# Kernel tuning notes

Measured on AMD Instinct MI355X. Metric: run time of the kernel, lower is better.

Reference implementation:

```python
import jax, jax.numpy as jnp
import numpy as np

B, T, D, H = 4, 2048, 512, 8
DH = D // H


def setup_inputs() -> dict:
    key = jax.random.key(0)
    ks = jax.random.split(key, 13)
    s = 1.0 / np.sqrt(D)
    inp = {
        "q": jax.random.normal(ks[0], (B, T, D), jnp.float32),
        "k": jax.random.normal(ks[1], (B, T, D), jnp.float32),
        "v": jax.random.normal(ks[2], (B, T, D), jnp.float32),
        # key padding mask, broadcastable to [B, H, T_q, T_k]; mostly True
        "padding_mask": jax.random.uniform(ks[3], (B, 1, 1, T)) > 0.1,
        "W_q": jax.random.normal(ks[4], (D, D), jnp.float32) * s,
        "b_q": jnp.zeros((D,), jnp.float32),
        "W_k": jax.random.normal(ks[5], (D, D), jnp.float32) * s,
        "b_k": jnp.zeros((D,), jnp.float32),
        "W_v": jax.random.normal(ks[6], (D, D), jnp.float32) * s,
        "b_v": jnp.zeros((D,), jnp.float32),
        "W_o": jax.random.normal(ks[7], (D, D), jnp.float32) * s,
        "b_o": jnp.zeros((D,), jnp.float32),
    }
    return inp


def reference(q, k, v, padding_mask, W_q, b_q, W_k, b_k, W_v, b_v, W_o, b_o):
    # Linear projections, then split heads: [B, T, D] -> [B, H, T, DH]
    def heads(x, W, b):
        y = x @ W + b
        return y.reshape(x.shape[0], x.shape[1], H, DH).transpose(0, 2, 1, 3)

    Q = heads(q, W_q, b_q)
    K = heads(k, W_k, b_k)
    V = heads(v, W_v, b_v)

    scores = jnp.einsum("bhqd,bhkd->bhqk", Q, K) / jnp.sqrt(jnp.float32(DH))
    scores = jnp.where(padding_mask, scores, -jnp.inf)
    weights = jax.nn.softmax(scores, axis=-1)
    weights = jnp.nan_to_num(weights, nan=0.0)  # all-masked rows -> 0
    x = jnp.einsum("bhqk,bhkd->bhqd", weights, V)
    x = x.transpose(0, 2, 1, 3).reshape(q.shape[0], q.shape[1], D)
    return x @ W_o + b_o
```

## Files before the change

### kernel.cpp

```cpp
#include <hip/hip_runtime.h>
#include <hip/hip_bf16.h>
#include <math.h>


#define TB 2048
#define DD 512
#define NH 8
#define DH 64

typedef short bf16x8 __attribute__((ext_vector_type(8)));
typedef float f32x4 __attribute__((ext_vector_type(4)));

static __device__ __forceinline__ ushort f2bf(float x) {
  __hip_bfloat16 h = __float2bfloat16(x);
  return *reinterpret_cast<ushort*>(&h);
}
static __device__ __forceinline__ float bf2f(ushort u) {
  unsigned int v = ((unsigned int)u) << 16;
  return __uint_as_float(v);
}
static __device__ __forceinline__ float fast_exp2(float x) {
  return __builtin_amdgcn_exp2f(x);
}
static __device__ __forceinline__ unsigned pack2(float x, float y) {
  return __builtin_amdgcn_perm(__float_as_uint(y) + 0x8000u,
                               __float_as_uint(x) + 0x8000u, 0x07060302u);
}
static __device__ __forceinline__ bf16x8 cvt8(float4 lo, float4 hi) {
  union { unsigned u[4]; bf16x8 v; } r;
  r.u[0] = pack2(lo.x, lo.y);
  r.u[1] = pack2(lo.z, lo.w);
  r.u[2] = pack2(hi.x, hi.y);
  r.u[3] = pack2(hi.z, hi.w);
  return r.v;
}

__global__ void mask_detect_kernel(const unsigned char* __restrict__ m,
                                   int* __restrict__ mode) {
  __shared__ int c1, c2;
  if (threadIdx.x == 0) { c1 = 0; c2 = 0; }
  __syncthreads();
  int l1 = 0, l2 = 0;
  for (int i = threadIdx.x; i < 8192; i += blockDim.x) {
    int ph = i & 3;
    unsigned char v = m[i];
    if (ph == 1 && v) l1++;
    if (ph == 2 && v) l2++;
  }
  if (l1) atomicAdd(&c1, l1);
  if (l2) atomicAdd(&c2, l2);
  __syncthreads();
  if (threadIdx.x == 0) *mode = (c1 > 0) ? 0 : ((c2 > 0) ? 1 : 2);
}

__global__ void mask_build_kernel(const void* __restrict__ m,
                                  const int* __restrict__ mode,
                                  float* __restrict__ out) {
  int i = blockIdx.x * blockDim.x + threadIdx.x;
  int md = *mode;
  int v;
  if (md == 0)      v = ((const unsigned char*)m)[i] != 0;
  else if (md == 1) v = ((const float*)m)[i] != 0.0f;
  else              v = ((const int*)m)[i] != 0;
  out[i] = v ? 0.0f : -INFINITY;
}

__global__ __launch_bounds__(256) void wtrans3_kernel(
    const float* __restrict__ Wq, const float* __restrict__ Wk,
    const float* __restrict__ Wv, ushort* __restrict__ Wall) {
  __shared__ ushort t[64][68];
  const float* W = (blockIdx.z == 0) ? Wq : (blockIdx.z == 1) ? Wk : Wv;
  ushort* Wt = Wall + (size_t)blockIdx.z * (512 * 512);
  const int bn = blockIdx.x << 6, bk = blockIdx.y << 6;
  const int tx = threadIdx.x & 15, ty = threadIdx.x >> 4;
#pragma unroll
  for (int rr = 0; rr < 64; rr += 16) {
    float4 v = *(const float4*)&W[(size_t)(bk + rr + ty) * DD + bn + (tx << 2)];
    t[(tx << 2) + 0][rr + ty] = f2bf(v.x);
    t[(tx << 2) + 1][rr + ty] = f2bf(v.y);
    t[(tx << 2) + 2][rr + ty] = f2bf(v.z);
    t[(tx << 2) + 3][rr + ty] = f2bf(v.w);
  }
  __syncthreads();
#pragma unroll
  for (int rr = 0; rr < 64; rr += 16) {
    ushort4 o;
    o.x = t[rr + ty][(tx << 2) + 0];
    o.y = t[rr + ty][(tx << 2) + 1];
    o.z = t[rr + ty][(tx << 2) + 2];
    o.w = t[rr + ty][(tx << 2) + 3];
    *(ushort4*)&Wt[(size_t)(bn + rr + ty) * DD + bk + (tx << 2)] = o;
  }
}

__global__ __launch_bounds__(256) void wtrans_split_kernel(
    const float* __restrict__ W, ushort* __restrict__ Wt) {
  __shared__ ushort thi[64][68];
  __shared__ ushort tlo[64][68];
  const int bn = blockIdx.x << 6, bk = blockIdx.y << 6;
  const int tx = threadIdx.x & 15, ty = threadIdx.x >> 4;
#pragma unroll
  for (int rr = 0; rr < 64; rr += 16) {
    float4 v = *(const float4*)&W[(size_t)(bk + rr + ty) * DD + bn + (tx << 2)];
    float vv[4] = {v.x, v.y, v.z, v.w};
#pragma unroll
    for (int c = 0; c < 4; ++c) {
      ushort hi = f2bf(vv[c]);
      ushort lo = f2bf(vv[c] - bf2f(hi));
      thi[(tx << 2) + c][rr + ty] = hi;
      tlo[(tx << 2) + c][rr + ty] = lo;
    }
  }
  __syncthreads();
#pragma unroll
  for (int rr = 0; rr < 64; rr += 16) {
    ushort4 h4, l4;
    h4.x = thi[rr + ty][(tx << 2) + 0];
    h4.y = thi[rr + ty][(tx << 2) + 1];
    h4.z = thi[rr + ty][(tx << 2) + 2];
    h4.w = thi[rr + ty][(tx << 2) + 3];
    l4.x = tlo[rr + ty][(tx << 2) + 0];
    l4.y = tlo[rr + ty][(tx << 2) + 1];
    l4.z = tlo[rr + ty][(tx << 2) + 2];
    l4.w = tlo[rr + ty][(tx << 2) + 3];
    size_t rowb = (size_t)(bn + rr + ty) * 1536;
    *(ushort4*)&Wt[rowb + bk + (tx << 2)] = h4;
    *(ushort4*)&Wt[rowb + 512 + bk + (tx << 2)] = h4;
    *(ushort4*)&Wt[rowb + 1024 + bk + (tx << 2)] = l4;
  }
}

__global__ __launch_bounds__(256) void projqkv_kernel(
    const float* __restrict__ Qx, const float* __restrict__ Kx,
    const float* __restrict__ Vx, const ushort* __restrict__ Wall,
    const float* __restrict__ bq, const float* __restrict__ bk,
    const float* __restrict__ bv, ushort* __restrict__ Yall, float qscale) {
  __shared__ __align__(16) ushort As[2][128][32];
  __shared__ __align__(16) ushort Bs[2][128][32];

  const int tid = threadIdx.x;
  const int w = tid >> 6, lane = tid & 63;
  const int llo = lane & 15, lhi = lane >> 4;
  const int wm = w >> 1, wn = w & 1;

  const int bid = blockIdx.x;
  const int x = bid & 7, rest = bid >> 3;
  const int ni = rest & 3;
  const int gg = (rest >> 2) * 8 + x;
  const int sec = gg >> 6;
  const int mt = gg & 63;
  const int m0 = mt << 7;
  const int n0s = ni << 7;

  const float* A = (sec == 0) ? Qx : (sec == 1) ? Kx : Vx;
  const float* bias = (sec == 0) ? bq : (sec == 1) ? bk : bv;
  const float scale = (sec == 0) ? qscale : 1.0f;
  const ushort* Wt = Wall + (size_t)(sec * 512 + n0s) * DD;

  const int srow = tid >> 1, scol = (tid & 1) << 4;
  const float* Ag = A + (size_t)(m0 + srow) * DD + scol;
  const ushort* Bg = Wt + (size_t)srow * DD + scol;

  f32x4 acc[4][4];
#pragma unroll
  for (int mi = 0; mi < 4; ++mi)
#pragma unroll
    for (int nj = 0; nj < 4; ++nj) acc[mi][nj] = (f32x4){0.f, 0.f, 0.f, 0.f};

  {
    float4 f0 = *(const float4*)(Ag + 0);
    float4 f1 = *(const float4*)(Ag + 4);
    float4 f2 = *(const float4*)(Ag + 8);
    float4 f3 = *(const float4*)(Ag + 12);
    bf16x8 w0 = *(const bf16x8*)(Bg + 0);
    bf16x8 w1 = *(const bf16x8*)(Bg + 8);
    *(bf16x8*)&As[0][srow][scol] = cvt8(f0, f1);
    *(bf16x8*)&As[0][srow][scol + 8] = cvt8(f2, f3);
    *(bf16x8*)&Bs[0][srow][scol] = w0;
    *(bf16x8*)&Bs[0][srow][scol + 8] = w1;
  }
  __syncthreads();

  int cur = 0;
  for (int t = 0; t < 16; ++t) {
    float4 f0, f1, f2, f3;
    bf16x8 w0, w1;
    if (t < 15) {
      const float* ag = Ag + (t + 1) * 32;
      const ushort* bg = Bg + (t + 1) * 32;
      f0 = *(const float4*)(ag + 0);
      f1 = *(const float4*)(ag + 4);
      f2 = *(const float4*)(ag + 8);
      f3 = *(const float4*)(ag + 12);
      w0 = *(const bf16x8*)(bg + 0);
      w1 = *(const bf16x8*)(bg + 8);
    }
    bf16x8 af[4], bfr[4];
#pragma unroll
    for (int mi = 0; mi < 4; ++mi)
      af[mi] = *(const bf16x8*)&As[cur][wm * 64 + mi * 16 + llo][lhi * 8];
#pragma unroll
    for (int nj = 0; nj < 4; ++nj)
      bfr[nj] = *(const bf16x8*)&Bs[cur][wn * 64 + nj * 16 + llo][lhi * 8];
    __builtin_amdgcn_s_setprio(1);
#pragma unroll
    for (int mi = 0; mi < 4; ++mi)
#pragma unroll
      for (int nj = 0; nj < 4; ++nj)
        acc[mi][nj] = __builtin_amdgcn_mfma_f32_16x16x32_bf16(
            af[mi], bfr[nj], acc[mi][nj], 0, 0, 0);
    __builtin_amdgcn_s_setprio(0);
    if (t < 15) {
      *(bf16x8*)&As[cur ^ 1][srow][scol] = cvt8(f0, f1);
      *(bf16x8*)&As[cur ^ 1][srow][scol + 8] = cvt8(f2, f3);
      *(bf16x8*)&Bs[cur ^ 1][srow][scol] = w0;
      *(bf16x8*)&Bs[cur ^ 1][srow][scol + 8] = w1;
    }
    __syncthreads();
    cur ^= 1;
  }

  float bb[4];
#pragma unroll
  for (int nj = 0; nj < 4; ++nj)
    bb[nj] = bias[n0s + wn * 64 + nj * 16 + llo];

  ushort* Yq = Yall;
  ushort* Yk = Yall + ((size_t)4 << 20);
  ushort* Yv = Yall + ((size_t)8 << 20);
#pragma unroll
  for (int mi = 0; mi < 4; ++mi)
#pragma unroll
    for (int nj = 0; nj < 4; ++nj) {
      int colS = n0s + wn * 64 + nj * 16 + llo;
      int h = colS >> 6, dh = colS & (DH - 1);
#pragma unroll
      for (int r = 0; r < 4; ++r) {
        int row = m0 + wm * 64 + mi * 16 + lhi * 4 + r;
        int bidx = row >> 11, t = row & (TB - 1);
        int bh = bidx * NH + h;
        ushort u = f2bf((acc[mi][nj][r] + bb[nj]) * scale);
        if (sec == 0) {
          Yq[((size_t)(bh * 128 + (t >> 4)) * 2 + (dh >> 5)) * 512 +
             ((((dh >> 3) & 3) << 4) + (t & 15)) * 8 + (dh & 7)] = u;
        } else if (sec == 1) {
          Yk[((size_t)(bh * 32 + (t >> 6)) << 12) +
             (((dh >> 5) << 2) + ((t >> 4) & 3)) * 512 +
             ((((dh >> 3) & 3) << 4) + (t & 15)) * 8 + (dh & 7)] = u;
        } else {
          Yv[((size_t)(bh * 32 + (t >> 6)) << 12) +
             ((((t >> 5) & 1) << 2) + (dh >> 4)) * 512 +
             ((((t >> 3) & 3) << 4) + (dh & 15)) * 8 + (t & 7)] = u;
        }
      }
    }
}

__global__ __launch_bounds__(256) void projo_kernel(
    const ushort* __restrict__ A, const ushort* __restrict__ Wt,
    const float* __restrict__ bias, float* __restrict__ Y) {
  __shared__ __align__(16) ushort As[2][128][32];
  __shared__ __align__(16) ushort Bs[2][64][32];

  const int tid = threadIdx.x;
  const int w = tid >> 6, lane = tid & 63;
  const int llo = lane & 15, lhi = lane >> 4;
  const int wm = w >> 1, wn = w & 1;

  const int bid = blockIdx.x;
  const int x = bid & 7, rest = bid >> 3;
  const int ni = rest & 7;
  const int mt = (rest >> 3) * 8 + x;
  const int m0 = mt << 7;
  const int n0 = ni << 6;
  const int K = 1536;

  const int arow = tid >> 1, acol = (tid & 1) << 4;
  const int brow = tid >> 2, bcol = (tid & 3) << 3;
  const ushort* Ag = A + (size_t)(m0 + arow) * K + acol;
  const ushort* Bg = Wt + (size_t)(n0 + brow) * K + bcol;

  f32x4 acc[4][2];
#pragma unroll
  for (int mi = 0; mi < 4; ++mi)
#pragma unroll
    for (int nj = 0; nj < 2; ++nj) acc[mi][nj] = (f32x4){0.f, 0.f, 0.f, 0.f};

  {
    bf16x8 a0 = *(const bf16x8*)(Ag + 0);
    bf16x8 a1 = *(const bf16x8*)(Ag + 8);
    bf16x8 b0 = *(const bf16x8*)(Bg + 0);
    *(bf16x8*)&As[0][arow][acol] = a0;
    *(bf16x8*)&As[0][arow][acol + 8] = a1;
    *(bf16x8*)&Bs[0][brow][bcol] = b0;
  }
  __syncthreads();

  int cur = 0;
#pragma unroll 2
  for (int t = 0; t < 48; ++t) {
    bf16x8 a0, a1, b0;
    if (t < 47) {
      const ushort* ag = Ag + (t + 1) * 32;
      const ushort* bg = Bg + (t + 1) * 32;
      a0 = *(const bf16x8*)(ag + 0);
      a1 = *(const bf16x8*)(ag + 8);
      b0 = *(const bf16x8*)(bg + 0);
    }
    bf16x8 af[4], bfr[2];
#pragma unroll
    for (int mi = 0; mi < 4; ++mi)
      af[mi] = *(const bf16x8*)&As[cur][wm * 64 + mi * 16 + llo][lhi * 8];
#pragma unroll
    for (int nj = 0; nj < 2; ++nj)
      bfr[nj] = *(const bf16x8*)&Bs[cur][wn * 32 + nj * 16 + llo][lhi * 8];
    __builtin_amdgcn_s_setprio(1);
#pragma unroll
    for (int mi = 0; mi < 4; ++mi)
#pragma unroll
      for (int nj = 0; nj < 2; ++nj)
        acc[mi][nj] = __builtin_amdgcn_mfma_f32_16x16x32_bf16(
            af[mi], bfr[nj], acc[mi][nj], 0, 0, 0);
    __builtin_amdgcn_s_setprio(0);
    if (t < 47) {
      *(bf16x8*)&As[cur ^ 1][arow][acol] = a0;
      *(bf16x8*)&As[cur ^ 1][arow][acol + 8] = a1;
      *(bf16x8*)&Bs[cur ^ 1][brow][bcol] = b0;
    }
    __syncthreads();
    cur ^= 1;
  }

  float bb[2];
#pragma unroll
  for (int nj = 0; nj < 2; ++nj)
    bb[nj] = bias[n0 + wn * 32 + nj * 16 + llo];
#pragma unroll
  for (int mi = 0; mi < 4; ++mi)
#pragma unroll
    for (int nj = 0; nj < 2; ++nj) {
      int col = n0 + wn * 32 + nj * 16 + llo;
#pragma unroll
      for (int r = 0; r < 4; ++r) {
        int row = m0 + wm * 64 + mi * 16 + lhi * 4 + r;
        Y[(size_t)row * DD + col] = acc[mi][nj][r] + bb[nj];
      }
    }
}

__global__ __launch_bounds__(256) void attn_mfma_kernel(
    const ushort* __restrict__ Qf,
    const ushort* __restrict__ Kf,
    const ushort* __restrict__ Vf,
    const float* __restrict__ mbias,
    ushort* __restrict__ Ap) {
  __shared__ __align__(16) ushort Plds[4][2][16][72];

  const int tid = threadIdx.x;
  const int w = tid >> 6, lane = tid & 63;
  const int lhi = lane >> 4, llo = lane & 15;
  const int lane8 = lane * 8;

  const int bid = blockIdx.x;
  const int j = bid >> 3;
  const int bh = (bid & 7) + ((j >> 4) << 3);
  const int qt = j & 15;
  const int b = bh >> 3, h = bh & 7;
  const int q0 = qt << 7;

  const float* mb = mbias + b * TB;
  ushort* plA = &Plds[w][0][0][0];
  ushort* plB = &Plds[w][1][0][0];

  const ushort* Qb =
      Qf + ((size_t)((bh << 7) + (q0 >> 4) + w * 2) * 2) * 512 + lane8;
  bf16x8 qa0 = *(const bf16x8*)Qb;
  bf16x8 qa1 = *(const bf16x8*)(Qb + 512);
  bf16x8 qa2 = *(const bf16x8*)(Qb + 1024);
  bf16x8 qa3 = *(const bf16x8*)(Qb + 1536);

  const size_t bhK = (size_t)bh << 5;
  f32x4 oaccA[4], oaccB[4];
#pragma unroll
  for (int nt = 0; nt < 4; ++nt) {
    oaccA[nt] = (f32x4){0.f, 0.f, 0.f, 0.f};
    oaccB[nt] = (f32x4){0.f, 0.f, 0.f, 0.f};
  }
  float mA = -INFINITY, lA = 0.f;
  float mB = -INFINITY, lB = 0.f;

  for (int kt64 = 0; kt64 < 32; ++kt64) {
    const ushort* Kt = Kf + ((bhK + kt64) << 12) + lane8;
    bf16x8 kf[8];
#pragma unroll
    for (int i = 0; i < 8; ++i) kf[i] = *(const bf16x8*)(Kt + i * 512);
    float4 mb4[4];
#pragma unroll
    for (int nt = 0; nt < 4; ++nt)
      mb4[nt] = *(const float4*)&mb[kt64 * 64 + nt * 16 + lhi * 4];

    f32x4 sA[4], sB[4];
    __builtin_amdgcn_s_setprio(1);
#pragma unroll
    for (int nt = 0; nt < 4; ++nt) {
      sA[nt] = (f32x4){0.f, 0.f, 0.f, 0.f};
      sA[nt] = __builtin_amdgcn_mfma_f32_16x16x32_bf16(kf[nt], qa0, sA[nt], 0, 0, 0);
      sA[nt] = __builtin_amdgcn_mfma_f32_16x16x32_bf16(kf[4 + nt], qa1, sA[nt], 0, 0, 0);
    }
#pragma unroll
    for (int nt = 0; nt < 4; ++nt) {
      sB[nt] = (f32x4){0.f, 0.f, 0.f, 0.f};
      sB[nt] = __builtin_amdgcn_mfma_f32_16x16x32_bf16(kf[nt], qa2, sB[nt], 0, 0, 0);
      sB[nt] = __builtin_amdgcn_mfma_f32_16x16x32_bf16(kf[4 + nt], qa3, sB[nt], 0, 0, 0);
    }
    __builtin_amdgcn_s_setprio(0);

    const ushort* Vt = Vf + ((bhK + kt64) << 12) + lane8;
    bf16x8 vf[8];
#pragma unroll
    for (int i = 0; i < 8; ++i) vf[i] = *(const bf16x8*)(Vt + i * 512);

#pragma unroll
    for (int nt = 0; nt < 4; ++nt) {
      sA[nt][0] += mb4[nt].x; sB[nt][0] += mb4[nt].x;
      sA[nt][1] += mb4[nt].y; sB[nt][1] += mb4[nt].y;
      sA[nt][2] += mb4[nt].z; sB[nt][2] += mb4[nt].z;
      sA[nt][3] += mb4[nt].w; sB[nt][3] += mb4[nt].w;
    }

    {
      float mx0 = fmaxf(fmaxf(sA[0][0], sA[0][1]), fmaxf(sA[0][2], sA[0][3]));
      float mx1 = fmaxf(fmaxf(sA[1][0], sA[1][1]), fmaxf(sA[1][2], sA[1][3]));
      float mx2 = fmaxf(fmaxf(sA[2][0], sA[2][1]), fmaxf(sA[2][2], sA[2][3]));
      float mx3 = fmaxf(fmaxf(sA[3][0], sA[3][1]), fmaxf(sA[3][2], sA[3][3]));
      float lmax = fmaxf(fmaxf(mx0, mx1), fmaxf(mx2, mx3));
      if (__any(lmax > mA + 8.f)) {
        float rmax = fmaxf(lmax, __shfl_xor(lmax, 16));
        rmax = fmaxf(rmax, __shfl_xor(rmax, 32));
        float newm = fmaxf(mA, rmax);
        float alpha = (newm == -INFINITY) ? 0.f : fast_exp2(mA - newm);
        float al[4];
#pragma unroll
        for (int r = 0; r < 4; ++r) al[r] = __shfl(alpha, lhi * 4 + r);
#pragma unroll
        for (int nt = 0; nt < 4; ++nt) {
          oaccA[nt][0] *= al[0];
          oaccA[nt][1] *= al[1];
          oaccA[nt][2] *= al[2];
          oaccA[nt][3] *= al[3];
        }
        lA *= alpha;
        mA = newm;
      }
#pragma unroll
      for (int nt = 0; nt < 4; ++nt)
#pragma unroll
        for (int r = 0; r < 4; ++r) sA[nt][r] = fast_exp2(sA[nt][r] - mA);
      if (__any(mA == -INFINITY)) {
        if (mA == -INFINITY) {
#pragma unroll
          for (int nt = 0; nt < 4; ++nt) sA[nt] = (f32x4){0.f, 0.f, 0.f, 0.f};
        }
      }
      float s0 = (sA[0][0] + sA[0][1]) + (sA[0][2] + sA[0][3]);
      float s1 = (sA[1][0] + sA[1][1]) + (sA[1][2] + sA[1][3]);
      float s2 = (sA[2][0] + sA[2][1]) + (sA[2][2] + sA[2][3]);
      float s3 = (sA[3][0] + sA[3][1]) + (sA[3][2] + sA[3][3]);
      lA += (s0 + s1) + (s2 + s3);
#pragma unroll
      for (int nt = 0; nt < 4; ++nt) {
        unsigned int lo = pack2(sA[nt][0], sA[nt][1]);
        unsigned int hi = pack2(sA[nt][2], sA[nt][3]);
        *(uint2*)&plA[llo * 72 + nt * 16 + lhi * 4] = make_uint2(lo, hi);
      }
    }

    {
      float mx0 = fmaxf(fmaxf(sB[0][0], sB[0][1]), fmaxf(sB[0][2], sB[0][3]));
      float mx1 = fmaxf(fmaxf(sB[1][0], sB[1][1]), fmaxf(sB[1][2], sB[1][3]));
      float mx2 = fmaxf(fmaxf(sB[2][0], sB[2][1]), fmaxf(sB[2][2], sB[2][3]));
      float mx3 = fmaxf(fmaxf(sB[3][0], sB[3][1]), fmaxf(sB[3][2], sB[3][3]));
      float lmax = fmaxf(fmaxf(mx0, mx1), fmaxf(mx2, mx3));
      if (__any(lmax > mB + 8.f)) {
        float rmax = fmaxf(lmax, __shfl_xor(lmax, 16));
        rmax = fmaxf(rmax, __shfl_xor(rmax, 32));
        float newm = fmaxf(mB, rmax);
        float alpha = (newm == -INFINITY) ? 0.f : fast_exp2(mB - newm);
        float al[4];
#pragma unroll
        for (int r = 0; r < 4; ++r) al[r] = __shfl(alpha, lhi * 4 + r);
#pragma unroll
        for (int nt = 0; nt < 4; ++nt) {
          oaccB[nt][0] *= al[0];
          oaccB[nt][1] *= al[1];
          oaccB[nt][2] *= al[2];
          oaccB[nt][3] *= al[3];
        }
        lB *= alpha;
        mB = newm;
      }
#pragma unroll
      for (int nt = 0; nt < 4; ++nt)
#pragma unroll
        for (int r = 0; r < 4; ++r) sB[nt][r] = fast_exp2(sB[nt][r] - mB);
      if (__any(mB == -INFINITY)) {
        if (mB == -INFINITY) {
#pragma unroll
          for (int nt = 0; nt < 4; ++nt) sB[nt] = (f32x4){0.f, 0.f, 0.f, 0.f};
        }
      }
      float s0 = (sB[0][0] + sB[0][1]) + (sB[0][2] + sB[0][3]);
      float s1 = (sB[1][0] + sB[1][1]) + (sB[1][2] + sB[1][3]);
      float s2 = (sB[2][0] + sB[2][1]) + (sB[2][2] + sB[2][3]);
      float s3 = (sB[3][0] + sB[3][1]) + (sB[3][2] + sB[3][3]);
      lB += (s0 + s1) + (s2 + s3);
#pragma unroll
      for (int nt = 0; nt < 4; ++nt) {
        unsigned int lo = pack2(sB[nt][0], sB[nt][1]);
        unsigned int hi = pack2(sB[nt][2], sB[nt][3]);
        *(uint2*)&plB[llo * 72 + nt * 16 + lhi * 4] = make_uint2(lo, hi);
      }
    }

    __builtin_amdgcn_s_setprio(1);
#pragma unroll
    for (int kc = 0; kc < 2; ++kc) {
      bf16x8 paA = *(const bf16x8*)&plA[llo * 72 + kc * 32 + lhi * 8];
      bf16x8 paB = *(const bf16x8*)&plB[llo * 72 + kc * 32 + lhi * 8];
#pragma unroll
      for (int nt = 0; nt < 4; ++nt) {
        oaccA[nt] = __builtin_amdgcn_mfma_f32_16x16x32_bf16(paA, vf[kc * 4 + nt], oaccA[nt], 0, 0, 0);
        oaccB[nt] = __builtin_amdgcn_mfma_f32_16x16x32_bf16(paB, vf[kc * 4 + nt], oaccB[nt], 0, 0, 0);
      }
    }
    __builtin_amdgcn_s_setprio(0);
  }

  lA += __shfl_xor(lA, 16);
  lA += __shfl_xor(lA, 32);
  lB += __shfl_xor(lB, 16);
  lB += __shfl_xor(lB, 32);
  float invA = (lA > 0.f) ? 1.f / lA : 0.f;
  float invB = (lB > 0.f) ? 1.f / lB : 0.f;
  float ilA[4], ilB[4];
#pragma unroll
  for (int r = 0; r < 4; ++r) {
    ilA[r] = __shfl(invA, lhi * 4 + r);
    ilB[r] = __shfl(invB, lhi * 4 + r);
  }
  const int t0 = q0 + w * 32 + lhi * 4;
#pragma unroll
  for (int r = 0; r < 4; ++r) {
    size_t rowbA = (size_t)(b * TB + t0 + r) * 1536;
    size_t rowbB = (size_t)(b * TB + t0 + 16 + r) * 1536;
#pragma unroll
    for (int nt = 0; nt < 4; ++nt) {
      int c = h * DH + nt * 16 + llo;
      float oA = oaccA[nt][r] * ilA[r];
      ushort hiA = f2bf(oA);
      ushort loA = f2bf(oA - bf2f(hiA));
      Ap[rowbA + c] = hiA;
      Ap[rowbA + 512 + c] = loA;
      Ap[rowbA + 1024 + c] = hiA;
      float oB = oaccB[nt][r] * ilB[r];
      ushort hiB = f2bf(oB);
      ushort loB = f2bf(oB - bf2f(hiB));
      Ap[rowbB + c] = hiB;
      Ap[rowbB + 512 + c] = loB;
      Ap[rowbB + 1024 + c] = hiB;
    }
  }
}

extern "C" void kernel_launch(void* const* d_in, const int* in_sizes, int n_in,
                              void* d_out, int out_size, void* d_ws,
                              size_t ws_size, hipStream_t stream) {
  (void)in_sizes; (void)n_in; (void)out_size; (void)ws_size;
  const float* q = (const float*)d_in[0];
  const float* k = (const float*)d_in[1];
  const float* v = (const float*)d_in[2];
  const void* pm = d_in[3];
  const float* Wq = (const float*)d_in[4];
  const float* bq = (const float*)d_in[5];
  const float* Wk = (const float*)d_in[6];
  const float* bk = (const float*)d_in[7];
  const float* Wv = (const float*)d_in[8];
  const float* bv = (const float*)d_in[9];
  const float* Wo = (const float*)d_in[10];
  const float* bo = (const float*)d_in[11];

  char* ws = (char*)d_ws;
  const size_t MB = (size_t)1 << 20;
  ushort* Ap = (ushort*)(ws);
  ushort* Wall = (ushort*)(ws + 24 * MB);
  ushort* Wot = (ushort*)(ws + 26 * MB);
  ushort* Qh = (ushort*)(ws + 32 * MB);
  float* mbias = (float*)(ws + 56 * MB);
  int* mode = (int*)(ws + 56 * MB + 40960);

  mask_detect_kernel<<<1, 256, 0, stream>>>((const unsigned char*)pm, mode);
  mask_build_kernel<<<32, 256, 0, stream>>>(pm, mode, mbias);

  wtrans3_kernel<<<dim3(8, 8, 3), 256, 0, stream>>>(Wq, Wk, Wv, Wall);
  wtrans_split_kernel<<<dim3(8, 8), 256, 0, stream>>>(Wo, Wot);

  const float qscale = 0.125f * 1.4426950408889634f;
  projqkv_kernel<<<768, 256, 0, stream>>>(q, k, v, Wall,
                                          bq, bk, bv, Qh, qscale);

  attn_mfma_kernel<<<512, 256, 0, stream>>>(
      Qh, Qh + ((size_t)4 << 20), Qh + ((size_t)8 << 20), mbias, Ap);

  projo_kernel<<<512, 256, 0, stream>>>(Ap, Wot, bo, (float*)d_out);
}
```

Baseline: 142.1 us.

## Stage K/V tiles in double-buffered LDS shared across waves, fold mask into MFMA

Previously each of the four waves loaded the full K and V tile for every 64-key step straight from global memory, so every tile was read four times per block. Now all 256 threads cooperatively load each tile once into a double-buffered LDS buffer, prefetching the next tile into registers while the current one is computed on. The mask bias is also passed as the MFMA accumulator input, which removes the separate add. This costs extra LDS (32 KB) and a block-wide barrier per step, which may lower occupancy and add synchronisation stalls.

```diff
diff --git a/kernel.cpp b/kernel.cpp
--- a/kernel.cpp
+++ b/kernel.cpp
@@ -354,12 +354,14 @@
     const ushort* __restrict__ Vf,
     const float* __restrict__ mbias,
     ushort* __restrict__ Ap) {
+  __shared__ __align__(16) ushort KV[2][2][4096];
   __shared__ __align__(16) ushort Plds[4][2][16][72];
 
   const int tid = threadIdx.x;
   const int w = tid >> 6, lane = tid & 63;
   const int lhi = lane >> 4, llo = lane & 15;
   const int lane8 = lane * 8;
+  const int st16 = tid * 16;
 
   const int bid = blockIdx.x;
   const int j = bid >> 3;
@@ -389,44 +391,62 @@
   float mA = -INFINITY, lA = 0.f;
   float mB = -INFINITY, lB = 0.f;
 
+  {
+    const ushort* Kt = Kf + (bhK << 12) + st16;
+    const ushort* Vt = Vf + (bhK << 12) + st16;
+    bf16x8 k0 = *(const bf16x8*)Kt;
+    bf16x8 k1 = *(const bf16x8*)(Kt + 8);
+    bf16x8 v0 = *(const bf16x8*)Vt;
+    bf16x8 v1 = *(const bf16x8*)(Vt + 8);
+    *(bf16x8*)&KV[0][0][st16] = k0;
+    *(bf16x8*)&KV[0][0][st16 + 8] = k1;
+    *(bf16x8*)&KV[0][1][st16] = v0;
+    *(bf16x8*)&KV[0][1][st16 + 8] = v1;
+  }
+  __syncthreads();
+
+  int cur = 0;
   for (int kt64 = 0; kt64 < 32; ++kt64) {
-    const ushort* Kt = Kf + ((bhK + kt64) << 12) + lane8;
-    bf16x8 kf[8];
-#pragma unroll
-    for (int i = 0; i < 8; ++i) kf[i] = *(const bf16x8*)(Kt + i * 512);
+    bf16x8 nk0, nk1, nv0, nv1;
+    if (kt64 < 31) {
+      const ushort* Kt = Kf + ((bhK + kt64 + 1) << 12) + st16;
+      const ushort* Vt = Vf + ((bhK + kt64 + 1) << 12) + st16;
+      nk0 = *(const bf16x8*)Kt;
+      nk1 = *(const bf16x8*)(Kt + 8);
+      nv0 = *(const bf16x8*)Vt;
+      nv1 = *(const bf16x8*)(Vt + 8);
+    }
+
     float4 mb4[4];
 #pragma unroll
     for (int nt = 0; nt < 4; ++nt)
       mb4[nt] = *(const float4*)&mb[kt64 * 64 + nt * 16 + lhi * 4];
 
+    bf16x8 kf[8];
+#pragma unroll
+    for (int i = 0; i < 8; ++i)
+      kf[i] = *(const bf16x8*)&KV[cur][0][i * 512 + lane8];
+
     f32x4 sA[4], sB[4];
     __builtin_amdgcn_s_setprio(1);
 #pragma unroll
     for (int nt = 0; nt < 4; ++nt) {
-      sA[nt] = (f32x4){0.f, 0.f, 0.f, 0.f};
-      sA[nt] = __builtin_amdgcn_mfma_f32_16x16x32_bf16(kf[nt], qa0, sA[nt], 0, 0, 0);
+      f32x4 ci = (f32x4){mb4[nt].x, mb4[nt].y, mb4[nt].z, mb4[nt].w};
+      sA[nt] = __builtin_amdgcn_mfma_f32_16x16x32_bf16(kf[nt], qa0, ci, 0, 0, 0);
       sA[nt] = __builtin_amdgcn_mfma_f32_16x16x32_bf16(kf[4 + nt], qa1, sA[nt], 0, 0, 0);
     }
 #pragma unroll
     for (int nt = 0; nt < 4; ++nt) {
-      sB[nt] = (f32x4){0.f, 0.f, 0.f, 0.f};
-      sB[nt] = __builtin_amdgcn_mfma_f32_16x16x32_bf16(kf[nt], qa2, sB[nt], 0, 0, 0);
+      f32x4 ci = (f32x4){mb4[nt].x, mb4[nt].y, mb4[nt].z, mb4[nt].w};
+      sB[nt] = __builtin_amdgcn_mfma_f32_16x16x32_bf16(kf[nt], qa2, ci, 0, 0, 0);
       sB[nt] = __builtin_amdgcn_mfma_f32_16x16x32_bf16(kf[4 + nt], qa3, sB[nt], 0, 0, 0);
     }
     __builtin_amdgcn_s_setprio(0);
 
-    const ushort* Vt = Vf + ((bhK + kt64) << 12) + lane8;
     bf16x8 vf[8];
 #pragma unroll
-    for (int i = 0; i < 8; ++i) vf[i] = *(const bf16x8*)(Vt + i * 512);
-
-#pragma unroll
-    for (int nt = 0; nt < 4; ++nt) {
-      sA[nt][0] += mb4[nt].x; sB[nt][0] += mb4[nt].x;
-      sA[nt][1] += mb4[nt].y; sB[nt][1] += mb4[nt].y;
-      sA[nt][2] += mb4[nt].z; sB[nt][2] += mb4[nt].z;
-      sA[nt][3] += mb4[nt].w; sB[nt][3] += mb4[nt].w;
-    }
+    for (int i = 0; i < 8; ++i)
+      vf[i] = *(const bf16x8*)&KV[cur][1][i * 512 + lane8];
 
     {
       float mx0 = fmaxf(fmaxf(sA[0][0], sA[0][1]), fmaxf(sA[0][2], sA[0][3]));
@@ -534,6 +554,15 @@
       }
     }
     __builtin_amdgcn_s_setprio(0);
+
+    if (kt64 < 31) {
+      *(bf16x8*)&KV[cur ^ 1][0][st16] = nk0;
+      *(bf16x8*)&KV[cur ^ 1][0][st16 + 8] = nk1;
+      *(bf16x8*)&KV[cur ^ 1][1][st16] = nv0;
+      *(bf16x8*)&KV[cur ^ 1][1][st16 + 8] = nv1;
+    }
+    __syncthreads();
+    cur ^= 1;
   }
 
   lA += __shfl_xor(lA, 16);
```

Measured after the change: 146.2 us. +2.9%, slower.
